# Performance work log

Measured on AMD Instinct MI355X. Metric: run time of the kernel, lower is better.

## Reference

```python
import jax, jax.numpy as jnp
import numpy as np

B, T, D, H, Dh, ROT = 2, 2048, 2048, 16, 128, 64
DFF = 4 * D
EPS = 1e-5
NEG = -1e9


def setup_inputs() -> dict:
    key = jax.random.key(0)
    ks = jax.random.split(key, 8)
    s = lambda k, shape, sc: jax.random.normal(k, shape, jnp.float32) * sc
    return {
        "x": s(ks[0], (B, T, D), 1.0),
        "ln_scale": jnp.ones((D,), jnp.float32),
        "ln_offset": jnp.zeros((D,), jnp.float32),
        "wq": s(ks[1], (D, D), 0.02),
        "wk": s(ks[2], (D, D), 0.02),
        "wv": s(ks[3], (D, D), 0.02),
        "wo": s(ks[4], (D, D), 0.02),
        "w1": s(ks[5], (D, DFF), 0.02),
        "b1": jnp.zeros((DFF,), jnp.float32),
        "w2": s(ks[6], (DFF, D), 0.02),
        "b2": jnp.zeros((D,), jnp.float32),
    }


def reference(x, ln_scale, ln_offset, wq, wk, wv, wo, w1, b1, w2, b2):
    def ln(h):  # ReplicatedLayerNorm, fp32 internal; note: same params used twice (shared self.norm)
        h32 = h.astype(jnp.float32)
        m = jnp.mean(h32, axis=-1, keepdims=True)
        v = jnp.var(h32, axis=-1, keepdims=True)
        y = (h32 - m) * jax.lax.rsqrt(v + EPS)
        return (y * ln_scale + ln_offset).astype(h.dtype)

    xn = ln(x)
    q = (xn @ wq).reshape(B, T, H, Dh)
    k = (xn @ wk).reshape(B, T, H, Dh)
    v = (xn @ wv).reshape(B, T, H, Dh)

    # GPT-J interleaved RoPE on first ROT dims
    pos = jnp.arange(T, dtype=jnp.float32)
    inv_freq = 1.0 / (10000.0 ** (jnp.arange(0, ROT, 2, dtype=jnp.float32) / ROT))
    freqs = pos[:, None] * inv_freq[None, :]            # (T, ROT/2)
    cos = jnp.repeat(jnp.cos(freqs), 2, axis=-1)[None, :, None, :]  # (1,T,1,ROT)
    sin = jnp.repeat(jnp.sin(freqs), 2, axis=-1)[None, :, None, :]

    def rope(t):
        tr, tp = t[..., :ROT], t[..., ROT:]
        x1 = tr[..., 0::2]
        x2 = tr[..., 1::2]
        rot_half = jnp.stack((-x2, x1), axis=-1).reshape(tr.shape)
        return jnp.concatenate([tr * cos + rot_half * sin, tp], axis=-1)

    q, k = rope(q), rope(k)

    scale = 1.0 / jnp.sqrt(jnp.float32(Dh))
    scores = jnp.einsum('bthd,bshd->bhts', q, k) * scale
    mask = jnp.where(jnp.tril(jnp.ones((T, T), bool)), 0.0, NEG).astype(scores.dtype)
    w = jax.nn.softmax(scores + mask, axis=-1)
    ctx = jnp.einsum('bhts,bshd->bthd', w, v).reshape(B, T, D)
    x1_ = x + ctx @ wo

    xn2 = ln(x1_)
    h = jax.nn.gelu(xn2.astype(jnp.float32) @ w1 + b1)  # default approximate gelu, as in source
    ff = (h @ w2 + b2).astype(x.dtype)
    return x1_ + ff
```

## Files before the change

### kernel.cpp

```cpp
#include <hip/hip_runtime.h>
#include <hip/hip_bf16.h>

#define B_   2
#define T_   2048
#define D_   2048
#define H_   16
#define DH_  128
#define DFF_ 8192

typedef __attribute__((ext_vector_type(8))) short bf16x8;
typedef __attribute__((ext_vector_type(4))) float f32x4;

__device__ __forceinline__ short f2bf(float f) {
    __hip_bfloat16 h = __float2bfloat16(f);
    return *reinterpret_cast<short*>(&h);
}

__device__ __forceinline__ void gload_lds16(const void* g, void* l) {
    __builtin_amdgcn_global_load_lds(
        (const __attribute__((address_space(1))) void*)g,
        (__attribute__((address_space(3))) void*)l,
        16, 0, 0);
}

__device__ __forceinline__ float gelu_tanh(float x) {
    float x3 = x * x * x;
    return 0.5f * x * (1.f + tanhf(0.7978845608028654f * (x + 0.044715f * x3)));
}

#define MFMA32(a, b, c) __builtin_amdgcn_mfma_f32_16x16x32_bf16((a), (b), (c), 0, 0, 0)

__global__ __launch_bounds__(256) void transpose_cvt(const float* __restrict__ in,
                                                     __hip_bfloat16* __restrict__ out,
                                                     int K, int N, int out_ld, int out_row0)
{
    __shared__ float t[32][65];
    const int n0 = blockIdx.x * 64, k0 = blockIdx.y * 32;
    const int tid = threadIdx.x;
    {
        int kr = tid >> 4;
        int nc = (tid & 15) * 4;
        const float* src = in + (size_t)(k0 + kr) * N + n0 + nc;
        float4 a = *reinterpret_cast<const float4*>(src);
        float4 b = *reinterpret_cast<const float4*>(src + (size_t)16 * N);
        t[kr][nc] = a.x; t[kr][nc + 1] = a.y; t[kr][nc + 2] = a.z; t[kr][nc + 3] = a.w;
        t[kr + 16][nc] = b.x; t[kr + 16][nc + 1] = b.y; t[kr + 16][nc + 2] = b.z; t[kr + 16][nc + 3] = b.w;
    }
    __syncthreads();
    {
        int n  = tid >> 2;
        int kc = (tid & 3) * 8;
        __hip_bfloat16 ob[8];
#pragma unroll
        for (int j = 0; j < 8; ++j) ob[j] = __float2bfloat16(t[kc + j][n]);
        *reinterpret_cast<uint4*>(out + (size_t)(out_row0 + n0 + n) * out_ld + k0 + kc) =
            *reinterpret_cast<uint4*>(ob);
    }
}

__global__ __launch_bounds__(256) void ln_kernel(const float* __restrict__ x,
                                                 const float* __restrict__ sc,
                                                 const float* __restrict__ of,
                                                 __hip_bfloat16* __restrict__ out)
{
    int row = blockIdx.x, tid = threadIdx.x;
    const float* xr = x + (size_t)row * D_;
    float4 v0 = reinterpret_cast<const float4*>(xr)[tid * 2];
    float4 v1 = reinterpret_cast<const float4*>(xr)[tid * 2 + 1];
    float vv[8] = {v0.x, v0.y, v0.z, v0.w, v1.x, v1.y, v1.z, v1.w};
    float s = 0.f, ss = 0.f;
#pragma unroll
    for (int j = 0; j < 8; ++j) { s += vv[j]; ss += vv[j] * vv[j]; }
    for (int o = 32; o; o >>= 1) { s += __shfl_down(s, o); ss += __shfl_down(ss, o); }
    __shared__ float red[8];
    int wid = tid >> 6, lane = tid & 63;
    if (!lane) { red[wid] = s; red[4 + wid] = ss; }
    __syncthreads();
    s  = red[0] + red[1] + red[2] + red[3];
    ss = red[4] + red[5] + red[6] + red[7];
    float mean = s * (1.f / D_);
    float var  = ss * (1.f / D_) - mean * mean;
    float rstd = rsqrtf(var + 1e-5f);
    int c0 = tid * 8;
    __hip_bfloat16 ob[8];
#pragma unroll
    for (int j = 0; j < 8; ++j)
        ob[j] = __float2bfloat16((vv[j] - mean) * rstd * sc[c0 + j] + of[c0 + j]);
    *reinterpret_cast<uint4*>(out + (size_t)row * D_ + c0) = *reinterpret_cast<uint4*>(ob);
}

template<int EPI, int BM>
__global__ __launch_bounds__(512, 2) void gemm8p(
    const __hip_bfloat16* __restrict__ A, const __hip_bfloat16* __restrict__ BT,
    void* __restrict__ Cout, const float* __restrict__ bias,
    const float* __restrict__ resid, int M, int N, int K)
{
    constexpr int MFR = BM / 32;
    constexpr int AUL = BM / 128;
    constexpr int VMC = AUL + 2;
    __shared__ short As[2 * 2 * BM * 32];
    __shared__ short Bs[2 * 2 * 256 * 32];

    const int tid = threadIdx.x;
    const int wid = tid >> 6, lane = tid & 63;
    const int lo = lane & 15, hi = lane >> 4;
    const int wr = wid >> 2, wc = wid & 3;

    const int gx = gridDim.x;
    const int nwg = gx * gridDim.y;
    const int bid = blockIdx.y * gx + blockIdx.x;
    const int swz = (bid & 7) * (nwg >> 3) + (bid >> 3);
    const int m0 = (swz / gx) * BM, n0 = (swz % gx) * 256;

    auto stageA = [&](int tt, int ks) {
#pragma unroll
        for (int l = 0; l < AUL; ++l) {
            int c    = l * 512 + tid;
            int row  = c >> 2, ksub = c & 3;
            int kc   = tt * 64 + ks * 32 + ((ksub ^ ((row >> 1) & 3)) << 3);
            int c0   = l * 512 + wid * 64;
            gload_lds16(A + (size_t)(m0 + row) * K + kc,
                        (char*)As + ((tt & 1) * 2 + ks) * (BM * 64) + c0 * 16);
        }
    };
    auto stageB = [&](int tt, int ks) {
#pragma unroll
        for (int l = 0; l < 2; ++l) {
            int c    = l * 512 + tid;
            int row  = c >> 2, ksub = c & 3;
            int kc   = tt * 64 + ks * 32 + ((ksub ^ ((row >> 1) & 3)) << 3);
            int c0   = l * 512 + wid * 64;
            gload_lds16(BT + (size_t)(n0 + row) * K + kc,
                        (char*)Bs + ((tt & 1) * 2 + ks) * 16384 + c0 * 16);
        }
    };

    const int fsw  = (hi ^ ((lo >> 1) & 3)) << 4;
    const int arow = wr * (BM / 2) + lo;
    const int brow = wc * 64 + lo;

    f32x4 acc[MFR][4] = {};
    const int NT = K >> 6;

    stageA(0, 0); stageB(0, 0); stageA(0, 1); stageB(0, 1);
    asm volatile("s_waitcnt vmcnt(%0)" :: "i"(VMC) : "memory");
    __builtin_amdgcn_s_barrier();
    __builtin_amdgcn_sched_barrier(0);

#define PHASE_MFMA(J)                                                         \
        __builtin_amdgcn_s_barrier();                                         \
        asm volatile("s_waitcnt lgkmcnt(0)" ::: "memory");                    \
        __builtin_amdgcn_sched_barrier(0);                                    \
        __builtin_amdgcn_s_setprio(1);                                        \
        _Pragma("unroll")                                                     \
        for (int m = 0; m < MFR; ++m) {                                       \
            acc[m][J]     = MFMA32(af[m], b0, acc[m][J]);                     \
            acc[m][J + 1] = MFMA32(af[m], b1, acc[m][J + 1]);                 \
        }                                                                     \
        __builtin_amdgcn_s_setprio(0);

#pragma unroll 2
    for (int t = 0; t < NT; ++t) {
        const int bsel = t & 1;
        const bool pf = (t + 1 < NT);
        const char* Ab = (const char*)As + bsel * (2 * BM * 64);
        const char* Bb = (const char*)Bs + bsel * 32768;
        bf16x8 af[MFR], b0, b1;

#pragma unroll
        for (int m = 0; m < MFR; ++m)
            af[m] = *reinterpret_cast<const bf16x8*>(Ab + (arow + m * 16) * 64 + fsw);
        b0 = *reinterpret_cast<const bf16x8*>(Bb + brow * 64 + fsw);
        b1 = *reinterpret_cast<const bf16x8*>(Bb + (brow + 16) * 64 + fsw);
        if (pf) stageA(t + 1, 0);
        PHASE_MFMA(0)
        __builtin_amdgcn_s_barrier();
        __builtin_amdgcn_sched_barrier(0);

        b0 = *reinterpret_cast<const bf16x8*>(Bb + (brow + 32) * 64 + fsw);
        b1 = *reinterpret_cast<const bf16x8*>(Bb + (brow + 48) * 64 + fsw);
        if (pf) stageB(t + 1, 0);
        PHASE_MFMA(2)
        asm volatile("s_waitcnt vmcnt(%0)" :: "i"(VMC) : "memory");
        __builtin_amdgcn_s_barrier();
        __builtin_amdgcn_sched_barrier(0);

#pragma unroll
        for (int m = 0; m < MFR; ++m)
            af[m] = *reinterpret_cast<const bf16x8*>(Ab + BM * 64 + (arow + m * 16) * 64 + fsw);
        b0 = *reinterpret_cast<const bf16x8*>(Bb + 16384 + brow * 64 + fsw);
        b1 = *reinterpret_cast<const bf16x8*>(Bb + 16384 + (brow + 16) * 64 + fsw);
        if (pf) stageA(t + 1, 1);
        PHASE_MFMA(0)
        __builtin_amdgcn_s_barrier();
        __builtin_amdgcn_sched_barrier(0);

        b0 = *reinterpret_cast<const bf16x8*>(Bb + 16384 + (brow + 32) * 64 + fsw);
        b1 = *reinterpret_cast<const bf16x8*>(Bb + 16384 + (brow + 48) * 64 + fsw);
        if (pf) stageB(t + 1, 1);
        PHASE_MFMA(2)
        asm volatile("s_waitcnt vmcnt(%0)" :: "i"(VMC) : "memory");
        __builtin_amdgcn_s_barrier();
        __builtin_amdgcn_sched_barrier(0);
    }
#undef PHASE_MFMA

    float* Cf = (float*)Cout;
    __hip_bfloat16* Cb = (__hip_bfloat16*)Cout;
#pragma unroll
    for (int m = 0; m < MFR; ++m) {
        int rbase = m0 + wr * (BM / 2) + m * 16 + hi * 4;
#pragma unroll
        for (int j = 0; j < 4; ++j) {
            int col = n0 + wc * 64 + (j >> 1) * 32 + (j & 1) * 16 + lo;
            float bv = (EPI == 2 || EPI == 3) ? bias[col] : 0.f;
#pragma unroll
            for (int i = 0; i < 4; ++i) {
                size_t idx = (size_t)(rbase + i) * N + col;
                float v = acc[m][j][i];
                if (EPI == 2 || EPI == 3) v += bv;
                if (EPI == 2) v = gelu_tanh(v);
                if (EPI == 1 || EPI == 3) v += resid[idx];
                if (EPI == 0 || EPI == 2) Cb[idx] = __float2bfloat16(v);
                else                      Cf[idx] = v;
            }
        }
    }
}

__global__ __launch_bounds__(256) void rope_kernel(__hip_bfloat16* __restrict__ qkv)
{
    int idx = blockIdx.x * 256 + threadIdx.x;
    int p  = idx & 31;
    int h  = (idx >> 5) & (H_ - 1);
    int bt = idx >> 9;
    int t  = bt & (T_ - 1);
    float invf = exp2f((float)p * -0.4152410118609203f);
    float fr = (float)t * invf;
    float cs, sn;
    __sincosf(fr, &sn, &cs);
    size_t base = (size_t)bt * (3 * D_) + h * DH_ + 2 * p;
#pragma unroll
    for (int qk = 0; qk < 2; ++qk) {
        uint* pp = reinterpret_cast<uint*>(qkv + base + qk * D_);
        uint u = *pp;
        float x1 = __uint_as_float(u << 16);
        float x2 = __uint_as_float(u & 0xffff0000u);
        short r0 = f2bf(x1 * cs - x2 * sn);
        short r1 = f2bf(x2 * cs + x1 * sn);
        *pp = ((uint)(unsigned short)r0) | (((uint)(unsigned short)r1) << 16);
    }
}

__global__ __launch_bounds__(512) void attn_kernel(const __hip_bfloat16* __restrict__ qkv,
                                                   __hip_bfloat16* __restrict__ ctx)
{
    constexpr int LDQ = 3 * D_;
    constexpr int SV  = 68;

    int idx = blockIdx.y * 16 + blockIdx.x;
    int swz = (idx & 7) * 64 + (idx >> 3);
    const int bh  = swz >> 4;
    const int bxr = 15 - (swz & 15);
    const int b = bh >> 4, h = bh & 15;
    const int tq0 = bxr * 128;

    const int tid = threadIdx.x, wid = tid >> 6, lane = tid & 63;
    const int lo = lane & 15, hi = lane >> 4;
    const int t0 = tq0 + wid * 16;

    __shared__ short Ks[2][64 * 128];
    __shared__ short VsT[128 * SV];

    const __hip_bfloat16* qrow = qkv + (size_t)(b * T_ + t0 + lo) * LDQ + h * DH_;
    bf16x8 qf[4];
#pragma unroll
    for (int dk = 0; dk < 4; ++dk)
        qf[dk] = *reinterpret_cast<const bf16x8*>(qrow + dk * 32 + hi * 8);

    f32x4 octx[8] = {};
    float mreg = -1e30f, lreg = 0.f;

    const size_t kvrow0 = (size_t)(b * T_) * LDQ + h * DH_;
    const int nst = 2 * (bxr + 1);

    bf16x8 vr[2];

#define STAGE_K(s0v, buf)                                                     \
    do {                                                                      \
        _Pragma("unroll")                                                     \
        for (int i = 0; i < 2; ++i) {                                         \
            int c    = i * 512 + tid;                                         \
            int sr   = c >> 4;                                                \
            int cbs  = ((c & 15) * 16) ^ ((sr & 7) << 4);                     \
            gload_lds16(qkv + kvrow0 + (size_t)((s0v) + sr) * LDQ + D_ + (cbs >> 1), \
                        &Ks[buf][c * 8]);                                     \
        }                                                                     \
    } while (0)

#define LOAD_V(s0v)                                                           \
    do {                                                                      \
        _Pragma("unroll")                                                     \
        for (int it = 0; it < 2; ++it) {                                      \
            int c = it * 512 + tid;                                           \
            int s = c >> 4, dc = c & 15;                                      \
            vr[it] = *reinterpret_cast<const bf16x8*>(                        \
                qkv + kvrow0 + (size_t)((s0v) + s) * LDQ + 2 * D_ + dc * 8);  \
        }                                                                     \
    } while (0)

    STAGE_K(0, 0);
    LOAD_V(0);

    for (int st = 0; st < nst; ++st) {
        const int s0 = st * 64;
        const int cur = st & 1;
        __syncthreads();

#pragma unroll
        for (int it = 0; it < 2; ++it) {
            int c = it * 512 + tid;
            int s = c >> 4, dc = c & 15;
            int sswz = s ^ ((dc & 15) << 2);
            short* dst = &VsT[(dc * 8) * SV + sswz];
#pragma unroll
            for (int j = 0; j < 8; ++j)
                dst[j * SV] = vr[it][j];
        }
        if (st + 1 < nst) {
            STAGE_K(s0 + 64, cur ^ 1);
            LOAD_V(s0 + 64);
        }
        asm volatile("s_waitcnt lgkmcnt(0)" ::: "memory");
        __builtin_amdgcn_s_barrier();
        __builtin_amdgcn_sched_barrier(0);

        f32x4 sfr[4] = {};
        __builtin_amdgcn_s_setprio(1);
#pragma unroll
        for (int f = 0; f < 4; ++f) {
            int srow = f * 16 + lo;
            int sw = (srow & 7) << 4;
#pragma unroll
            for (int dk = 0; dk < 4; ++dk) {
                bf16x8 kf = *reinterpret_cast<const bf16x8*>(
                    (const char*)&Ks[cur][0] + srow * 256 + ((dk * 64 + hi * 16) ^ sw));
                sfr[f] = MFMA32(kf, qf[dk], sfr[f]);
            }
        }
        __builtin_amdgcn_s_setprio(0);

        const float qsc = 0.08838834764831845f;
#pragma unroll
        for (int f = 0; f < 4; ++f)
#pragma unroll
            for (int i = 0; i < 4; ++i)
                sfr[f][i] *= qsc;
        if (st >= nst - 2) {
#pragma unroll
            for (int f = 0; f < 4; ++f)
#pragma unroll
                for (int i = 0; i < 4; ++i)
                    if (s0 + f * 16 + hi * 4 + i > t0 + lo) sfr[f][i] = -1e30f;
        }

        float mx = -1e30f;
#pragma unroll
        for (int f = 0; f < 4; ++f)
#pragma unroll
            for (int i = 0; i < 4; ++i)
                mx = fmaxf(mx, sfr[f][i]);
        mx = fmaxf(mx, __shfl_xor(mx, 16));
        mx = fmaxf(mx, __shfl_xor(mx, 32));
        float mn = fmaxf(mreg, mx);
        float ps = __expf(mreg - mn);
        mreg = mn;
        float sum = 0.f;
#pragma unroll
        for (int f = 0; f < 4; ++f)
#pragma unroll
            for (int i = 0; i < 4; ++i) {
                sfr[f][i] = __expf(sfr[f][i] - mn);
                sum += sfr[f][i];
            }
        sum += __shfl_xor(sum, 16);
        sum += __shfl_xor(sum, 32);
        lreg = lreg * ps + sum;

        float psq[4];
#pragma unroll
        for (int i = 0; i < 4; ++i)
            psq[i] = __shfl(ps, hi * 4 + i);
#pragma unroll
        for (int f8 = 0; f8 < 8; ++f8)
#pragma unroll
            for (int i = 0; i < 4; ++i)
                octx[f8][i] *= psq[i];

#pragma unroll
        for (int ks = 0; ks < 2; ++ks) {
            union { bf16x8 v; short s[8]; } pa;
#pragma unroll
            for (int j = 0; j < 4; ++j) {
                pa.s[j]     = f2bf(sfr[2 * ks][j]);
                pa.s[j + 4] = f2bf(sfr[2 * ks + 1][j]);
            }
            __builtin_amdgcn_s_setprio(1);
#pragma unroll
            for (int f8 = 0; f8 < 8; ++f8) {
                int d = f8 * 16 + lo;
                int sw2 = ((d >> 3) & 15) << 2;
                const short* vrow = &VsT[d * SV];
                union { bf16x8 v; uint2 u[2]; } vb;
                vb.u[0] = *reinterpret_cast<const uint2*>(vrow + ((ks * 32 + hi * 4) ^ sw2));
                vb.u[1] = *reinterpret_cast<const uint2*>(vrow + ((ks * 32 + 16 + hi * 4) ^ sw2));
                octx[f8] = MFMA32(pa.v, vb.v, octx[f8]);
            }
            __builtin_amdgcn_s_setprio(0);
        }
    }
#undef STAGE_K
#undef LOAD_V

    float linv[4];
#pragma unroll
    for (int i = 0; i < 4; ++i)
        linv[i] = 1.f / __shfl(lreg, hi * 4 + i);
#pragma unroll
    for (int i = 0; i < 4; ++i) {
        size_t rb = (size_t)(b * T_ + t0 + hi * 4 + i) * D_ + h * DH_;
#pragma unroll
        for (int f8 = 0; f8 < 8; ++f8)
            ctx[rb + f8 * 16 + lo] = __float2bfloat16(octx[f8][i] * linv[i]);
    }
}

extern "C" void kernel_launch(void* const* d_in, const int* in_sizes, int n_in,
                              void* d_out, int out_size, void* d_ws, size_t ws_size,
                              hipStream_t stream)
{
    (void)in_sizes; (void)n_in; (void)out_size; (void)ws_size;
    const float* x   = (const float*)d_in[0];
    const float* lns = (const float*)d_in[1];
    const float* lno = (const float*)d_in[2];
    const float* wq  = (const float*)d_in[3];
    const float* wk  = (const float*)d_in[4];
    const float* wv  = (const float*)d_in[5];
    const float* wo  = (const float*)d_in[6];
    const float* w1  = (const float*)d_in[7];
    const float* b1  = (const float*)d_in[8];
    const float* w2  = (const float*)d_in[9];
    const float* b2  = (const float*)d_in[10];
    float* out = (float*)d_out;

    char* ws = (char*)d_ws;
    __hip_bfloat16* wqkvT = (__hip_bfloat16*)(ws);
    __hip_bfloat16* woT   = (__hip_bfloat16*)(ws + 25165824);
    __hip_bfloat16* w1T   = (__hip_bfloat16*)(ws + 33554432);
    __hip_bfloat16* w2T   = (__hip_bfloat16*)(ws + 67108864);
    __hip_bfloat16* xn    = (__hip_bfloat16*)(ws + 100663296);
    __hip_bfloat16* qkv   = (__hip_bfloat16*)(ws + 117440512);
    __hip_bfloat16* hbuf  = qkv;
    __hip_bfloat16* ctx   = (__hip_bfloat16*)(ws + 167772160);
    float*          x1    = (float*)(ws + 184549376);

    transpose_cvt<<<dim3(32, 64),  256, 0, stream>>>(wq, wqkvT, 2048, 2048, 2048, 0);
    transpose_cvt<<<dim3(32, 64),  256, 0, stream>>>(wk, wqkvT, 2048, 2048, 2048, 2048);
    transpose_cvt<<<dim3(32, 64),  256, 0, stream>>>(wv, wqkvT, 2048, 2048, 2048, 4096);
    transpose_cvt<<<dim3(32, 64),  256, 0, stream>>>(wo, woT,   2048, 2048, 2048, 0);
    transpose_cvt<<<dim3(128, 64), 256, 0, stream>>>(w1, w1T,   2048, 8192, 2048, 0);
    transpose_cvt<<<dim3(32, 256), 256, 0, stream>>>(w2, w2T,   8192, 2048, 8192, 0);

    ln_kernel<<<4096, 256, 0, stream>>>(x, lns, lno, xn);
    gemm8p<0, 128><<<dim3(24, 32), 512, 0, stream>>>(xn, wqkvT, qkv, nullptr, nullptr, 4096, 6144, 2048);
    rope_kernel<<<8192, 256, 0, stream>>>(qkv);
    attn_kernel<<<dim3(16, 32), 512, 0, stream>>>(qkv, ctx);
    gemm8p<1, 128><<<dim3(8, 32), 512, 0, stream>>>(ctx, woT, x1, nullptr, x, 4096, 2048, 2048);
    ln_kernel<<<4096, 256, 0, stream>>>(x1, lns, lno, xn);
    gemm8p<2, 256><<<dim3(32, 16), 512, 0, stream>>>(xn, w1T, hbuf, b1, nullptr, 4096, 8192, 2048);
    gemm8p<3, 128><<<dim3(8, 32), 512, 0, stream>>>(hbuf, w2T, out, b2, x1, 4096, 2048, 8192);
}
```

Measured before the change: 769.6 us.

## Add three-stage LDS pipeline to GEMM for BM=128 launches

Templates the GEMM on the number of shared-memory stages and adds a three-slot ring buffer that prefetches two k-tiles ahead. It waits on the older tile's loads only once per iteration instead of twice, aiming to hide more global-load latency. The BM=128 GEMMs (QKV, out-proj, FFN2) use three stages; the BM=256 FFN1 keeps two. LDS grows to 144KB per block, which at two blocks per CU under launch_bounds(512,2) may exceed the 160KB LDS per CU on MI355X and cut occupancy.

New measurement: 777.1 us. Within noise of the previous version (+1.0%).

```diff
diff --git a/kernel.cpp b/kernel.cpp
--- a/kernel.cpp
+++ b/kernel.cpp
@@ -89,7 +89,7 @@
     *reinterpret_cast<uint4*>(out + (size_t)row * D_ + c0) = *reinterpret_cast<uint4*>(ob);
 }
 
-template<int EPI, int BM>
+template<int EPI, int BM, int NS>
 __global__ __launch_bounds__(512, 2) void gemm8p(
     const __hip_bfloat16* __restrict__ A, const __hip_bfloat16* __restrict__ BT,
     void* __restrict__ Cout, const float* __restrict__ bias,
@@ -98,8 +98,9 @@
     constexpr int MFR = BM / 32;
     constexpr int AUL = BM / 128;
     constexpr int VMC = AUL + 2;
-    __shared__ short As[2 * 2 * BM * 32];
-    __shared__ short Bs[2 * 2 * 256 * 32];
+    constexpr int VMT = 2 * AUL + 4;
+    __shared__ short As[NS * 2 * BM * 32];
+    __shared__ short Bs[NS * 2 * 256 * 32];
 
     const int tid = threadIdx.x;
     const int wid = tid >> 6, lane = tid & 63;
@@ -112,7 +113,7 @@
     const int swz = (bid & 7) * (nwg >> 3) + (bid >> 3);
     const int m0 = (swz / gx) * BM, n0 = (swz % gx) * 256;
 
-    auto stageA = [&](int tt, int ks) {
+    auto stageA = [&](int tt, int ks, int slot) {
 #pragma unroll
         for (int l = 0; l < AUL; ++l) {
             int c    = l * 512 + tid;
@@ -120,10 +121,10 @@
             int kc   = tt * 64 + ks * 32 + ((ksub ^ ((row >> 1) & 3)) << 3);
             int c0   = l * 512 + wid * 64;
             gload_lds16(A + (size_t)(m0 + row) * K + kc,
-                        (char*)As + ((tt & 1) * 2 + ks) * (BM * 64) + c0 * 16);
+                        (char*)As + (slot * 2 + ks) * (BM * 64) + c0 * 16);
         }
     };
-    auto stageB = [&](int tt, int ks) {
+    auto stageB = [&](int tt, int ks, int slot) {
 #pragma unroll
         for (int l = 0; l < 2; ++l) {
             int c    = l * 512 + tid;
@@ -131,7 +132,7 @@
             int kc   = tt * 64 + ks * 32 + ((ksub ^ ((row >> 1) & 3)) << 3);
             int c0   = l * 512 + wid * 64;
             gload_lds16(BT + (size_t)(n0 + row) * K + kc,
-                        (char*)Bs + ((tt & 1) * 2 + ks) * 16384 + c0 * 16);
+                        (char*)Bs + (slot * 2 + ks) * 16384 + c0 * 16);
         }
     };
 
@@ -141,11 +142,6 @@
 
     f32x4 acc[MFR][4] = {};
     const int NT = K >> 6;
-
-    stageA(0, 0); stageB(0, 0); stageA(0, 1); stageB(0, 1);
-    asm volatile("s_waitcnt vmcnt(%0)" :: "i"(VMC) : "memory");
-    __builtin_amdgcn_s_barrier();
-    __builtin_amdgcn_sched_barrier(0);
 
 #define PHASE_MFMA(J)                                                         \
         __builtin_amdgcn_s_barrier();                                         \
@@ -159,49 +155,110 @@
         }                                                                     \
         __builtin_amdgcn_s_setprio(0);
 
-#pragma unroll 2
-    for (int t = 0; t < NT; ++t) {
-        const int bsel = t & 1;
-        const bool pf = (t + 1 < NT);
-        const char* Ab = (const char*)As + bsel * (2 * BM * 64);
-        const char* Bb = (const char*)Bs + bsel * 32768;
-        bf16x8 af[MFR], b0, b1;
-
-#pragma unroll
-        for (int m = 0; m < MFR; ++m)
-            af[m] = *reinterpret_cast<const bf16x8*>(Ab + (arow + m * 16) * 64 + fsw);
-        b0 = *reinterpret_cast<const bf16x8*>(Bb + brow * 64 + fsw);
-        b1 = *reinterpret_cast<const bf16x8*>(Bb + (brow + 16) * 64 + fsw);
-        if (pf) stageA(t + 1, 0);
-        PHASE_MFMA(0)
-        __builtin_amdgcn_s_barrier();
-        __builtin_amdgcn_sched_barrier(0);
-
-        b0 = *reinterpret_cast<const bf16x8*>(Bb + (brow + 32) * 64 + fsw);
-        b1 = *reinterpret_cast<const bf16x8*>(Bb + (brow + 48) * 64 + fsw);
-        if (pf) stageB(t + 1, 0);
-        PHASE_MFMA(2)
+    if constexpr (NS == 2) {
+        stageA(0, 0, 0); stageB(0, 0, 0); stageA(0, 1, 0); stageB(0, 1, 0);
         asm volatile("s_waitcnt vmcnt(%0)" :: "i"(VMC) : "memory");
         __builtin_amdgcn_s_barrier();
         __builtin_amdgcn_sched_barrier(0);
 
-#pragma unroll
-        for (int m = 0; m < MFR; ++m)
-            af[m] = *reinterpret_cast<const bf16x8*>(Ab + BM * 64 + (arow + m * 16) * 64 + fsw);
-        b0 = *reinterpret_cast<const bf16x8*>(Bb + 16384 + brow * 64 + fsw);
-        b1 = *reinterpret_cast<const bf16x8*>(Bb + 16384 + (brow + 16) * 64 + fsw);
-        if (pf) stageA(t + 1, 1);
-        PHASE_MFMA(0)
+#pragma unroll 2
+        for (int t = 0; t < NT; ++t) {
+            const int bsel = t & 1;
+            const bool pf = (t + 1 < NT);
+            const char* Ab = (const char*)As + bsel * (2 * BM * 64);
+            const char* Bb = (const char*)Bs + bsel * 32768;
+            bf16x8 af[MFR], b0, b1;
+
+#pragma unroll
+            for (int m = 0; m < MFR; ++m)
+                af[m] = *reinterpret_cast<const bf16x8*>(Ab + (arow + m * 16) * 64 + fsw);
+            b0 = *reinterpret_cast<const bf16x8*>(Bb + brow * 64 + fsw);
+            b1 = *reinterpret_cast<const bf16x8*>(Bb + (brow + 16) * 64 + fsw);
+            if (pf) stageA(t + 1, 0, bsel ^ 1);
+            PHASE_MFMA(0)
+            __builtin_amdgcn_s_barrier();
+            __builtin_amdgcn_sched_barrier(0);
+
+            b0 = *reinterpret_cast<const bf16x8*>(Bb + (brow + 32) * 64 + fsw);
+            b1 = *reinterpret_cast<const bf16x8*>(Bb + (brow + 48) * 64 + fsw);
+            if (pf) stageB(t + 1, 0, bsel ^ 1);
+            PHASE_MFMA(2)
+            asm volatile("s_waitcnt vmcnt(%0)" :: "i"(VMC) : "memory");
+            __builtin_amdgcn_s_barrier();
+            __builtin_amdgcn_sched_barrier(0);
+
+#pragma unroll
+            for (int m = 0; m < MFR; ++m)
+                af[m] = *reinterpret_cast<const bf16x8*>(Ab + BM * 64 + (arow + m * 16) * 64 + fsw);
+            b0 = *reinterpret_cast<const bf16x8*>(Bb + 16384 + brow * 64 + fsw);
+            b1 = *reinterpret_cast<const bf16x8*>(Bb + 16384 + (brow + 16) * 64 + fsw);
+            if (pf) stageA(t + 1, 1, bsel ^ 1);
+            PHASE_MFMA(0)
+            __builtin_amdgcn_s_barrier();
+            __builtin_amdgcn_sched_barrier(0);
+
+            b0 = *reinterpret_cast<const bf16x8*>(Bb + 16384 + (brow + 32) * 64 + fsw);
+            b1 = *reinterpret_cast<const bf16x8*>(Bb + 16384 + (brow + 48) * 64 + fsw);
+            if (pf) stageB(t + 1, 1, bsel ^ 1);
+            PHASE_MFMA(2)
+            asm volatile("s_waitcnt vmcnt(%0)" :: "i"(VMC) : "memory");
+            __builtin_amdgcn_s_barrier();
+            __builtin_amdgcn_sched_barrier(0);
+        }
+    } else {
+        stageA(0, 0, 0); stageB(0, 0, 0); stageA(0, 1, 0); stageB(0, 1, 0);
+        stageA(1, 0, 1); stageB(1, 0, 1); stageA(1, 1, 1); stageB(1, 1, 1);
+        asm volatile("s_waitcnt vmcnt(%0)" :: "i"(VMT) : "memory");
         __builtin_amdgcn_s_barrier();
         __builtin_amdgcn_sched_barrier(0);
 
-        b0 = *reinterpret_cast<const bf16x8*>(Bb + 16384 + (brow + 32) * 64 + fsw);
-        b1 = *reinterpret_cast<const bf16x8*>(Bb + 16384 + (brow + 48) * 64 + fsw);
-        if (pf) stageB(t + 1, 1);
-        PHASE_MFMA(2)
-        asm volatile("s_waitcnt vmcnt(%0)" :: "i"(VMC) : "memory");
-        __builtin_amdgcn_s_barrier();
-        __builtin_amdgcn_sched_barrier(0);
+        int sC = 0;
+#pragma unroll 3
+        for (int t = 0; t < NT; ++t) {
+            const bool pf = (t + 2 < NT);
+            const int sS = (sC + 2 >= 3) ? sC - 1 : sC + 2;
+            const char* Ab = (const char*)As + sC * (2 * BM * 64);
+            const char* Bb = (const char*)Bs + sC * 32768;
+            bf16x8 af[MFR], b0, b1;
+
+#pragma unroll
+            for (int m = 0; m < MFR; ++m)
+                af[m] = *reinterpret_cast<const bf16x8*>(Ab + (arow + m * 16) * 64 + fsw);
+            b0 = *reinterpret_cast<const bf16x8*>(Bb + brow * 64 + fsw);
+            b1 = *reinterpret_cast<const bf16x8*>(Bb + (brow + 16) * 64 + fsw);
+            if (pf) stageA(t + 2, 0, sS);
+            PHASE_MFMA(0)
+            __builtin_amdgcn_s_barrier();
+            __builtin_amdgcn_sched_barrier(0);
+
+            b0 = *reinterpret_cast<const bf16x8*>(Bb + (brow + 32) * 64 + fsw);
+            b1 = *reinterpret_cast<const bf16x8*>(Bb + (brow + 48) * 64 + fsw);
+            if (pf) stageB(t + 2, 0, sS);
+            PHASE_MFMA(2)
+            __builtin_amdgcn_s_barrier();
+            __builtin_amdgcn_sched_barrier(0);
+
+#pragma unroll
+            for (int m = 0; m < MFR; ++m)
+                af[m] = *reinterpret_cast<const bf16x8*>(Ab + BM * 64 + (arow + m * 16) * 64 + fsw);
+            b0 = *reinterpret_cast<const bf16x8*>(Bb + 16384 + brow * 64 + fsw);
+            b1 = *reinterpret_cast<const bf16x8*>(Bb + 16384 + (brow + 16) * 64 + fsw);
+            if (pf) stageA(t + 2, 1, sS);
+            PHASE_MFMA(0)
+            __builtin_amdgcn_s_barrier();
+            __builtin_amdgcn_sched_barrier(0);
+
+            b0 = *reinterpret_cast<const bf16x8*>(Bb + 16384 + (brow + 32) * 64 + fsw);
+            b1 = *reinterpret_cast<const bf16x8*>(Bb + 16384 + (brow + 48) * 64 + fsw);
+            if (pf) stageB(t + 2, 1, sS);
+            PHASE_MFMA(2)
+            if (pf) asm volatile("s_waitcnt vmcnt(%0)" :: "i"(VMT) : "memory");
+            else    asm volatile("s_waitcnt vmcnt(0)" ::: "memory");
+            __builtin_amdgcn_s_barrier();
+            __builtin_amdgcn_sched_barrier(0);
+
+            sC = (sC == 2) ? 0 : sC + 1;
+        }
     }
 #undef PHASE_MFMA
 
@@ -472,11 +529,11 @@
     transpose_cvt<<<dim3(32, 256), 256, 0, stream>>>(w2, w2T,   8192, 2048, 8192, 0);
 
     ln_kernel<<<4096, 256, 0, stream>>>(x, lns, lno, xn);
-    gemm8p<0, 128><<<dim3(24, 32), 512, 0, stream>>>(xn, wqkvT, qkv, nullptr, nullptr, 4096, 6144, 2048);
+    gemm8p<0, 128, 3><<<dim3(24, 32), 512, 0, stream>>>(xn, wqkvT, qkv, nullptr, nullptr, 4096, 6144, 2048);
     rope_kernel<<<8192, 256, 0, stream>>>(qkv);
     attn_kernel<<<dim3(16, 32), 512, 0, stream>>>(qkv, ctx);
-    gemm8p<1, 128><<<dim3(8, 32), 512, 0, stream>>>(ctx, woT, x1, nullptr, x, 4096, 2048, 2048);
+    gemm8p<1, 128, 3><<<dim3(8, 32), 512, 0, stream>>>(ctx, woT, x1, nullptr, x, 4096, 2048, 2048);
     ln_kernel<<<4096, 256, 0, stream>>>(x1, lns, lno, xn);
-    gemm8p<2, 256><<<dim3(32, 16), 512, 0, stream>>>(xn, w1T, hbuf, b1, nullptr, 4096, 8192, 2048);
-    gemm8p<3, 128><<<dim3(8, 32), 512, 0, stream>>>(hbuf, w2T, out, b2, x1, 4096, 2048, 8192);
-}
+    gemm8p<2, 256, 2><<<dim3(32, 16), 512, 0, stream>>>(xn, w1T, hbuf, b1, nullptr, 4096, 8192, 2048);
+    gemm8p<3, 128, 3><<<dim3(8, 32), 512, 0, stream>>>(hbuf, w2T, out, b2, x1, 4096, 2048, 8192);
+}
```
